# Performance work log

Measured on AMD Instinct MI355X. Metric: run time of the kernel, lower is better.

## Reference

```python
import jax, jax.numpy as jnp
import numpy as np

N = 1_000_000
H = 256
DIMS = [1, H, H, H, H]
N_LAYERS = 4  # 4 linear layers, sin activation after the first 3


def setup_inputs() -> dict:
    key = jax.random.key(0)
    ks = jax.random.split(key, 1 + 2 * N_LAYERS)
    d = {"x": jax.random.normal(ks[0], (N, 2), dtype=jnp.float32)}
    i = 1
    for pre in ("x", "t"):
        for l in range(N_LAYERS):
            lim = 1.0 / np.sqrt(DIMS[l])  # torch.nn.Linear default init range
            d[f"{pre}W{l}"] = jax.random.uniform(
                ks[i], (DIMS[l], DIMS[l + 1]), dtype=jnp.float32, minval=-lim, maxval=lim)
            d[f"{pre}b{l}"] = jnp.zeros((DIMS[l + 1],), dtype=jnp.float32)
            i += 1
    return d


def _mlp(h, params):
    # params: list of (W, b); sin activation after all but the last layer
    n = len(params)
    for idx, (W, b) in enumerate(params):
        h = h @ W + b
        if idx < n - 1:
            h = jnp.sin(h)
    return h


def reference(x, xW0, xb0, xW1, xb1, xW2, xb2, xW3, xb3,
              tW0, tb0, tW1, tb1, tW2, tb2, tW3, tb3):
    x_params = [(xW0, xb0), (xW1, xb1), (xW2, xb2), (xW3, xb3)]
    t_params = [(tW0, tb0), (tW1, tb1), (tW2, tb2), (tW3, tb3)]
    nx = _mlp(x[:, 0:1], x_params)  # [N, H]
    nt = _mlp(x[:, 1:2], t_params)  # [N, H]
    # diag(A @ B.T) == rowwise dot product; avoids the O(N^2) matmul
    even = jnp.sum(nx[:, 0::2] * nt[:, 0::2], axis=-1)  # [N]
    odd = jnp.sum(nx[:, 1::2] * nt[:, 1::2], axis=-1)   # [N]
    return jnp.stack([even, odd], axis=-1)  # [N, 2]
```

## Files before the change

kernel.cpp:

```cpp
#include <hip/hip_runtime.h>


typedef _Float16 f16x8 __attribute__((ext_vector_type(8)));
typedef _Float16 f16x4 __attribute__((ext_vector_type(4)));
typedef float f32x4 __attribute__((ext_vector_type(4)));

__device__ __forceinline__ int hswz(int m, int kbyte) {
    return m * 512 + ((((kbyte >> 4) ^ (m & 7)) & 31) << 4) + (kbyte & 15);
}

__device__ __forceinline__ void barrier_lds() {
    asm volatile("s_waitcnt lgkmcnt(0)" ::: "memory");
    __builtin_amdgcn_s_barrier();
}

__device__ __forceinline__ void stage_frag(const _Float16* g, _Float16* l) {
    __builtin_amdgcn_global_load_lds(
        (const __attribute__((address_space(1))) unsigned int*)g,
        (__attribute__((address_space(3))) unsigned int*)l,
        16, 0, 0);
}

__global__ void prepack(const float* __restrict__ xW1, const float* __restrict__ xW2,
                        const float* __restrict__ xW3, const float* __restrict__ tW1,
                        const float* __restrict__ tW2, const float* __restrict__ tW3,
                        _Float16* __restrict__ dst)
{
    int g = blockIdx.x * 256 + threadIdx.x;
    int L = g >> 16;
    int r = g & 65535;
    int j    = r & 7;
    int ln   = (r >> 3) & 15;
    int quad = (r >> 7) & 3;
    int nhi  = (r >> 9) & 15;
    int ks   = (r >> 13) & 1;
    int c    = (r >> 14) & 3;
    const float* W;
    switch (L) {
        case 0: W = xW1; break;
        case 1: W = xW2; break;
        case 2: W = xW3; break;
        case 3: W = tW1; break;
        case 4: W = tW2; break;
        default: W = tW3; break;
    }
    int n = nhi * 16 + ln;
    int k = c * 64 + ks * 32 + quad * 8 + j;
    dst[g] = (_Float16)W[k * 256 + n];
}


__device__ __forceinline__ void layer0_scalar(
    float xv, const float* __restrict__ W0, const float* __restrict__ b0,
    _Float16* __restrict__ hb, int tid)
{
    int m = tid >> 2;
    int q = tid & 3;
#pragma unroll
    for (int g = 0; g < 8; ++g) {
        int n0 = q * 64 + g * 8;
        f16x8 hv;
#pragma unroll
        for (int e = 0; e < 8; ++e) {
            float z = fmaf(xv, W0[n0 + e], b0[n0 + e]);
            hv[e] = (_Float16)__sinf(z);
        }
        *(f16x8*)((char*)hb + hswz(m, n0 * 2)) = hv;
    }
}

template<bool WRITE_H, bool HAS_NEXT>
__device__ __forceinline__ void gemm_layer(
    const _Float16* __restrict__ Wl,
    const _Float16* __restrict__ Wnext,
    const float* __restrict__ bias,
    _Float16* __restrict__ hb,
    _Float16* __restrict__ stg,
    f32x4 acc[4][4],
    int lane, int ln, int quad, int wave)
{
    f32x4 zero = {0.f, 0.f, 0.f, 0.f};
#pragma unroll
    for (int i = 0; i < 4; ++i)
#pragma unroll
        for (int j = 0; j < 4; ++j)
            acc[i][j] = zero;

#pragma unroll
    for (int g = 0; g < 8; ++g) {
        if (g < 7 || HAS_NEXT) {
            asm volatile("s_waitcnt lgkmcnt(0)" ::: "memory");
            _Float16* dst = stg + ((g + 1) & 1) * 2048;
            const _Float16* src = (g < 7)
                ? Wl + (g + 1) * 8192 + wave * 2048 + lane * 8
                : Wnext + wave * 2048 + lane * 8;
#pragma unroll
            for (int i = 0; i < 4; ++i)
                stage_frag(src + i * 512, dst + i * 512);
        }

        if (g == 7 && !HAS_NEXT)
            asm volatile("s_waitcnt vmcnt(0)" ::: "memory");
        else
            asm volatile("s_waitcnt vmcnt(4)" ::: "memory");

        f16x8 afr[4];
#pragma unroll
        for (int i = 0; i < 4; ++i)
            afr[i] = *(const f16x8*)(stg + (g & 1) * 2048 + i * 512 + lane * 8);

        f16x8 bfr[4];
#pragma unroll
        for (int j = 0; j < 4; ++j)
            bfr[j] = *(const f16x8*)((const char*)hb +
                                     hswz(16 * j + ln, g * 64 + quad * 16));

        __builtin_amdgcn_s_setprio(1);
#pragma unroll
        for (int i = 0; i < 4; ++i)
#pragma unroll
            for (int j = 0; j < 4; ++j)
                acc[i][j] = __builtin_amdgcn_mfma_f32_16x16x32_f16(
                    afr[i], bfr[j], acc[i][j], 0, 0, 0);
        __builtin_amdgcn_s_setprio(0);
    }

    barrier_lds();

    if (WRITE_H) {
#pragma unroll
        for (int i = 0; i < 4; ++i) {
            int nb = wave * 64 + 16 * i + quad * 4;
            f32x4 bv = *(const f32x4*)&bias[nb];
#pragma unroll
            for (int j = 0; j < 4; ++j) {
                f16x4 hv;
                hv[0] = (_Float16)__sinf(acc[i][j][0] + bv[0]);
                hv[1] = (_Float16)__sinf(acc[i][j][1] + bv[1]);
                hv[2] = (_Float16)__sinf(acc[i][j][2] + bv[2]);
                hv[3] = (_Float16)__sinf(acc[i][j][3] + bv[3]);
                *(f16x4*)((char*)hb + hswz(16 * j + ln, nb * 2)) = hv;
            }
        }
        barrier_lds();
    }
}

__global__ __launch_bounds__(256, 2)
void mlp_fused(const float* __restrict__ x,
               const float* __restrict__ xW0, const float* __restrict__ xb0,
               const float* __restrict__ xb1, const float* __restrict__ xb2,
               const float* __restrict__ xb3,
               const float* __restrict__ tW0, const float* __restrict__ tb0,
               const float* __restrict__ tb1, const float* __restrict__ tb2,
               const float* __restrict__ tb3,
               const _Float16* __restrict__ Wp,
               float* __restrict__ out)
{
    __shared__ __align__(16) _Float16 hbuf[64 * 256];
    __shared__ __align__(16) _Float16 stage[4][2][2048];
    __shared__ __align__(16) float    params[10 * 256];

    const int tid = threadIdx.x;
    const int lane = tid & 63;
    const int wave = tid >> 6;
    const int ln = lane & 15;
    const int quad = lane >> 4;
    const int row0 = blockIdx.x * 64;

    {
        const float* psrc[10] = {xW0, xb0, tW0, tb0, xb1, xb2, xb3, tb1, tb2, tb3};
#pragma unroll
        for (int s = 0; s < 10; ++s)
            params[s * 256 + tid] = psrc[s][tid];
    }
    const float2 xv2 = ((const float2*)x)[row0 + (tid >> 2)];
    barrier_lds();

    _Float16* stg = &stage[wave][0][0];
    f32x4 xacc[4][4], tacc[4][4];

#pragma unroll
    for (int i = 0; i < 4; ++i)
        stage_frag(Wp + wave * 2048 + lane * 8 + i * 512, stg + i * 512);

    layer0_scalar(xv2.x, &params[0], &params[256], hbuf, tid);
    barrier_lds();

    gemm_layer<true , true >(Wp + 0 * 65536, Wp + 1 * 65536, &params[4 * 256],
                             hbuf, stg, xacc, lane, ln, quad, wave);
    gemm_layer<true , true >(Wp + 1 * 65536, Wp + 2 * 65536, &params[5 * 256],
                             hbuf, stg, xacc, lane, ln, quad, wave);
    gemm_layer<false, true >(Wp + 2 * 65536, Wp + 3 * 65536, nullptr,
                             hbuf, stg, xacc, lane, ln, quad, wave);

    layer0_scalar(xv2.y, &params[2 * 256], &params[3 * 256], hbuf, tid);
    barrier_lds();

    gemm_layer<true , true >(Wp + 3 * 65536, Wp + 4 * 65536, &params[7 * 256],
                             hbuf, stg, tacc, lane, ln, quad, wave);
    gemm_layer<true , true >(Wp + 4 * 65536, Wp + 5 * 65536, &params[8 * 256],
                             hbuf, stg, tacc, lane, ln, quad, wave);
    gemm_layer<false, false>(Wp + 5 * 65536, nullptr, nullptr,
                             hbuf, stg, tacc, lane, ln, quad, wave);

    const float* xb3l = &params[6 * 256];
    const float* tb3l = &params[9 * 256];
    float ev[4] = {0.f, 0.f, 0.f, 0.f};
    float od[4] = {0.f, 0.f, 0.f, 0.f};
#pragma unroll
    for (int i = 0; i < 4; ++i) {
        int nb = wave * 64 + 16 * i + quad * 4;
        f32x4 xb = *(const f32x4*)&xb3l[nb];
        f32x4 tb = *(const f32x4*)&tb3l[nb];
#pragma unroll
        for (int j = 0; j < 4; ++j) {
            float a0 = xacc[i][j][0] + xb[0], c0 = tacc[i][j][0] + tb[0];
            float a1 = xacc[i][j][1] + xb[1], c1 = tacc[i][j][1] + tb[1];
            float a2 = xacc[i][j][2] + xb[2], c2 = tacc[i][j][2] + tb[2];
            float a3 = xacc[i][j][3] + xb[3], c3 = tacc[i][j][3] + tb[3];
            ev[j] += a0 * c0 + a2 * c2;
            od[j] += a1 * c1 + a3 * c3;
        }
    }
#pragma unroll
    for (int j = 0; j < 4; ++j) {
        ev[j] += __shfl_xor(ev[j], 16, 64);
        ev[j] += __shfl_xor(ev[j], 32, 64);
        od[j] += __shfl_xor(od[j], 16, 64);
        od[j] += __shfl_xor(od[j], 32, 64);
    }

    float* red = (float*)hbuf;
    if (lane < 16) {
#pragma unroll
        for (int j = 0; j < 4; ++j) {
            red[wave * 128 + j * 32 + lane * 2 + 0] = ev[j];
            red[wave * 128 + j * 32 + lane * 2 + 1] = od[j];
        }
    }
    __syncthreads();
    if (tid < 128) {
        int jj = tid >> 5, m16 = (tid >> 1) & 15, p = tid & 1;
        int base = jj * 32 + m16 * 2 + p;
        float s = red[base] + red[128 + base] + red[256 + base] + red[384 + base];
        out[(row0 + 16 * jj + m16) * 2 + p] = s;
    }
}

extern "C" void kernel_launch(void* const* d_in, const int* in_sizes, int n_in,
                              void* d_out, int out_size, void* d_ws, size_t ws_size,
                              hipStream_t stream)
{
    const float* x   = (const float*)d_in[0];
    const float* xW0 = (const float*)d_in[1];
    const float* xb0 = (const float*)d_in[2];
    const float* xW1 = (const float*)d_in[3];
    const float* xb1 = (const float*)d_in[4];
    const float* xW2 = (const float*)d_in[5];
    const float* xb2 = (const float*)d_in[6];
    const float* xW3 = (const float*)d_in[7];
    const float* xb3 = (const float*)d_in[8];
    const float* tW0 = (const float*)d_in[9];
    const float* tb0 = (const float*)d_in[10];
    const float* tW1 = (const float*)d_in[11];
    const float* tb1 = (const float*)d_in[12];
    const float* tW2 = (const float*)d_in[13];
    const float* tb2 = (const float*)d_in[14];
    const float* tW3 = (const float*)d_in[15];
    const float* tb3 = (const float*)d_in[16];

    _Float16* Wp = (_Float16*)d_ws;
    const int N = in_sizes[0] / 2;

    prepack<<<1536, 256, 0, stream>>>(xW1, xW2, xW3, tW1, tW2, tW3, Wp);
    mlp_fused<<<N / 64, 256, 0, stream>>>(x, xW0, xb0, xb1, xb2, xb3,
                                          tW0, tb0, tb1, tb2, tb3,
                                          Wp, (float*)d_out);
}
```

Measured before the change: 950.5 us.

## Load weight fragments straight into registers with two-stage prefetch

Removes the per-wave LDS staging of weight fragments via global_load_lds and instead loads the A fragments directly from global memory into registers. Two stages of fragments are prefetched, two k-steps ahead, and the prefetch carries across layers into the next weight matrix. This removes LDS traffic, LDS footprint and the lgkmcnt/vmcnt waits around staging, at the cost of 32 extra VGPRs for the double-buffered fragments. Under the 2-blocks-per-CU launch bound the added registers could cause spills, and the compiler now decides where to place the load waits.

```diff
diff --git a/kernel.cpp b/kernel.cpp
--- a/kernel.cpp
+++ b/kernel.cpp
@@ -12,13 +12,6 @@
 __device__ __forceinline__ void barrier_lds() {
     asm volatile("s_waitcnt lgkmcnt(0)" ::: "memory");
     __builtin_amdgcn_s_barrier();
-}
-
-__device__ __forceinline__ void stage_frag(const _Float16* g, _Float16* l) {
-    __builtin_amdgcn_global_load_lds(
-        (const __attribute__((address_space(1))) unsigned int*)g,
-        (__attribute__((address_space(3))) unsigned int*)l,
-        16, 0, 0);
 }
 
 __global__ void prepack(const float* __restrict__ xW1, const float* __restrict__ xW2,
@@ -75,8 +68,7 @@
     const _Float16* __restrict__ Wnext,
     const float* __restrict__ bias,
     _Float16* __restrict__ hb,
-    _Float16* __restrict__ stg,
-    f32x4 acc[4][4],
+    f32x4 acc[4][4], f16x8 afr[2][4],
     int lane, int ln, int quad, int wave)
 {
     f32x4 zero = {0.f, 0.f, 0.f, 0.f};
@@ -86,29 +78,10 @@
         for (int j = 0; j < 4; ++j)
             acc[i][j] = zero;
 
+    const _Float16* abase = Wl + wave * 2048 + lane * 8;
+
 #pragma unroll
     for (int g = 0; g < 8; ++g) {
-        if (g < 7 || HAS_NEXT) {
-            asm volatile("s_waitcnt lgkmcnt(0)" ::: "memory");
-            _Float16* dst = stg + ((g + 1) & 1) * 2048;
-            const _Float16* src = (g < 7)
-                ? Wl + (g + 1) * 8192 + wave * 2048 + lane * 8
-                : Wnext + wave * 2048 + lane * 8;
-#pragma unroll
-            for (int i = 0; i < 4; ++i)
-                stage_frag(src + i * 512, dst + i * 512);
-        }
-
-        if (g == 7 && !HAS_NEXT)
-            asm volatile("s_waitcnt vmcnt(0)" ::: "memory");
-        else
-            asm volatile("s_waitcnt vmcnt(4)" ::: "memory");
-
-        f16x8 afr[4];
-#pragma unroll
-        for (int i = 0; i < 4; ++i)
-            afr[i] = *(const f16x8*)(stg + (g & 1) * 2048 + i * 512 + lane * 8);
-
         f16x8 bfr[4];
 #pragma unroll
         for (int j = 0; j < 4; ++j)
@@ -121,8 +94,19 @@
 #pragma unroll
             for (int j = 0; j < 4; ++j)
                 acc[i][j] = __builtin_amdgcn_mfma_f32_16x16x32_f16(
-                    afr[i], bfr[j], acc[i][j], 0, 0, 0);
+                    afr[g & 1][i], bfr[j], acc[i][j], 0, 0, 0);
         __builtin_amdgcn_s_setprio(0);
+
+        if (g < 6) {
+#pragma unroll
+            for (int i = 0; i < 4; ++i)
+                afr[g & 1][i] = *(const f16x8*)(abase + (g + 2) * 8192 + i * 512);
+        } else if (HAS_NEXT) {
+#pragma unroll
+            for (int i = 0; i < 4; ++i)
+                afr[g & 1][i] = *(const f16x8*)(Wnext + (g - 6) * 8192 +
+                                                wave * 2048 + lane * 8 + i * 512);
+        }
     }
 
     barrier_lds();
@@ -158,7 +142,6 @@
                float* __restrict__ out)
 {
     __shared__ __align__(16) _Float16 hbuf[64 * 256];
-    __shared__ __align__(16) _Float16 stage[4][2][2048];
     __shared__ __align__(16) float    params[10 * 256];
 
     const int tid = threadIdx.x;
@@ -175,34 +158,37 @@
             params[s * 256 + tid] = psrc[s][tid];
     }
     const float2 xv2 = ((const float2*)x)[row0 + (tid >> 2)];
-    barrier_lds();
-
-    _Float16* stg = &stage[wave][0][0];
+
     f32x4 xacc[4][4], tacc[4][4];
-
-#pragma unroll
-    for (int i = 0; i < 4; ++i)
-        stage_frag(Wp + wave * 2048 + lane * 8 + i * 512, stg + i * 512);
+    f16x8 afr[2][4];
+
+#pragma unroll
+    for (int s = 0; s < 2; ++s)
+#pragma unroll
+        for (int i = 0; i < 4; ++i)
+            afr[s][i] = *(const f16x8*)(Wp + s * 8192 + wave * 2048 +
+                                        lane * 8 + i * 512);
+    barrier_lds();
 
     layer0_scalar(xv2.x, &params[0], &params[256], hbuf, tid);
     barrier_lds();
 
     gemm_layer<true , true >(Wp + 0 * 65536, Wp + 1 * 65536, &params[4 * 256],
-                             hbuf, stg, xacc, lane, ln, quad, wave);
+                             hbuf, xacc, afr, lane, ln, quad, wave);
     gemm_layer<true , true >(Wp + 1 * 65536, Wp + 2 * 65536, &params[5 * 256],
-                             hbuf, stg, xacc, lane, ln, quad, wave);
+                             hbuf, xacc, afr, lane, ln, quad, wave);
     gemm_layer<false, true >(Wp + 2 * 65536, Wp + 3 * 65536, nullptr,
-                             hbuf, stg, xacc, lane, ln, quad, wave);
+                             hbuf, xacc, afr, lane, ln, quad, wave);
 
     layer0_scalar(xv2.y, &params[2 * 256], &params[3 * 256], hbuf, tid);
     barrier_lds();
 
     gemm_layer<true , true >(Wp + 3 * 65536, Wp + 4 * 65536, &params[7 * 256],
-                             hbuf, stg, tacc, lane, ln, quad, wave);
+                             hbuf, tacc, afr, lane, ln, quad, wave);
     gemm_layer<true , true >(Wp + 4 * 65536, Wp + 5 * 65536, &params[8 * 256],
-                             hbuf, stg, tacc, lane, ln, quad, wave);
+                             hbuf, tacc, afr, lane, ln, quad, wave);
     gemm_layer<false, false>(Wp + 5 * 65536, nullptr, nullptr,
-                             hbuf, stg, tacc, lane, ln, quad, wave);
+                             hbuf, tacc, afr, lane, ln, quad, wave);
 
     const float* xb3l = &params[6 * 256];
     const float* tb3l = &params[9 * 256];
```

Result: faster. 870.4 us (-8.4%).
